# Kernel optimization log

Hardware: AMD Instinct MI355X
Metric: run time of the kernel (lower is better)

Reference implementation:

```python
import jax, jax.numpy as jnp
import numpy as np

B, S, H, NH = 2, 2048, 2048, 16
HD = H // NH
SCALE = 1.0 / np.sqrt(HD).astype(np.float32)


def setup_inputs() -> dict:
    key = jax.random.key(0)
    ks = jax.random.split(key, 10)
    std = 1.0 / np.sqrt(H)
    return {
        "x": jax.random.normal(ks[0], (B, S, H), dtype=jnp.float32),
        "attention_mask": jnp.zeros((B, 1, 1, S), dtype=jnp.float32),
        "Wq": jax.random.normal(ks[1], (H, H), dtype=jnp.float32) * std,
        "bq": jnp.zeros((H,), dtype=jnp.float32),
        "Wk": jax.random.normal(ks[2], (H, H), dtype=jnp.float32) * std,
        "bk": jnp.zeros((H,), dtype=jnp.float32),
        "Wv": jax.random.normal(ks[3], (H, H), dtype=jnp.float32) * std,
        "bv": jnp.zeros((H,), dtype=jnp.float32),
        "Wo": jax.random.normal(ks[4], (H, H), dtype=jnp.float32) * std,
        "bo": jnp.zeros((H,), dtype=jnp.float32),
    }


def _heads(t):
    # [B,S,H] -> [B,NH,S,HD]
    return t.reshape(B, S, NH, HD).transpose(0, 2, 1, 3)


def reference(x, attention_mask, Wq, bq, Wk, bk, Wv, bv, Wo, bo):
    q = _heads(x @ Wq.T + bq)
    k = _heads(x @ Wk.T + bk)
    v = _heads(x @ Wv.T + bv)
    scores = jnp.einsum("bhqd,bhkd->bhqk", q, k) * SCALE + attention_mask
    probs = jax.nn.softmax(scores, axis=-1)
    ctx = jnp.einsum("bhqk,bhkd->bhqd", probs, v)
    ctx = ctx.transpose(0, 2, 1, 3).reshape(B, S, H)
    return ctx @ Wo.T + bo
```

## Files before the change

kernel.cpp:

```cpp
#include <hip/hip_runtime.h>
#include <cstdint>
#include <cstddef>

#define B_   2
#define S_   2048
#define H_   2048
#define NH_  16
#define HD_  128
#define MM_  (B_ * S_)
#define K_   H_
#define SCALE_F 0.08838834764831845f
#define LOG2E_F 1.4426950408889634f
#define QSCALE_F (SCALE_F * LOG2E_F)

typedef __bf16 bf16_t;
typedef __attribute__((ext_vector_type(8))) __bf16 bf16x8;
typedef __attribute__((ext_vector_type(4))) float  f32x4;
typedef __attribute__((ext_vector_type(4))) float  floatx4;

static __device__ __forceinline__ f32x4 mfma_16x16x32(bf16x8 a, bf16x8 b, f32x4 c) {
  return __builtin_amdgcn_mfma_f32_16x16x32_bf16(a, b, c, 0, 0, 0);
}

static __device__ __forceinline__ void gl2lds16(const bf16_t* g, bf16_t* l) {
  __builtin_amdgcn_global_load_lds(
      (const __attribute__((address_space(1))) void*)g,
      (__attribute__((address_space(3))) void*)l, 16, 0, 0);
}

static __device__ __forceinline__ float exp2_hw(float x) {
  float r;
  asm("v_exp_f32 %0, %1" : "=v"(r) : "v"(x));
  return r;
}

__global__ void cvt6_f32_bf16(const float* __restrict__ x,
                              const float* __restrict__ w0, const float* __restrict__ w1,
                              const float* __restrict__ w2, const float* __restrict__ w3,
                              bf16_t* xo, bf16_t* o0, bf16_t* o1, bf16_t* o2, bf16_t* o3,
                              int n8) {
  const int yy = blockIdx.y;
  const float* in;
  bf16_t* out;
  if (yy == 0)      { in = x;                      out = xo; }
  else if (yy == 1) { in = x + (size_t)H_ * H_;    out = xo + (size_t)H_ * H_; }
  else if (yy == 2) { in = w0; out = o0; }
  else if (yy == 3) { in = w1; out = o1; }
  else if (yy == 4) { in = w2; out = o2; }
  else              { in = w3; out = o3; }
  int i = blockIdx.x * blockDim.x + threadIdx.x;
  const int stride = gridDim.x * blockDim.x;
  for (; i < n8; i += stride) {
    const floatx4* p = (const floatx4*)(in + (size_t)i * 8);
    floatx4 a = p[0], b = p[1];
    bf16x8 o;
    o[0] = (bf16_t)a.x; o[1] = (bf16_t)a.y; o[2] = (bf16_t)a.z; o[3] = (bf16_t)a.w;
    o[4] = (bf16_t)b.x; o[5] = (bf16_t)b.y; o[6] = (bf16_t)b.z; o[7] = (bf16_t)b.w;
    *(bf16x8*)(out + (size_t)i * 8) = o;
  }
}

template <int MODE, int NCOLS>
__global__ __launch_bounds__(256) void gemm_bt(
    const bf16_t* __restrict__ A,
    const bf16_t* __restrict__ W0, const bf16_t* __restrict__ W1, const bf16_t* __restrict__ W2,
    const float* __restrict__ bias0, const float* __restrict__ bias1, const float* __restrict__ bias2,
    bf16_t* __restrict__ dq, bf16_t* __restrict__ dk, bf16_t* __restrict__ dv,
    float* __restrict__ outf)
{
  __shared__ __align__(16) bf16_t Ash[128 * 32];
  __shared__ __align__(16) bf16_t Bsh[128 * 32];

  const int t = threadIdx.x;
  const int lane = t & 63;
  const int wid  = t >> 6;
  const int wm = wid >> 1, wn = wid & 1;

  const int lin = blockIdx.x;
  const int xcd = lin & 7;
  const int loc = lin >> 3;
  const int sr  = loc >> 5;
  const int l   = loc & 31;
  const int r_  = xcd * (NCOLS / 8) + sr;
  const int tm  = (r_ & 3) * 8 + (l & 7);
  const int nc  = (r_ >> 2) * 4 + (l >> 3);
  const int bm  = tm * 128;

  int bn;
  int wsel = 0;
  const bf16_t* Bw;
  const float*  bias;
  bf16_t* dsth = nullptr;
  if constexpr (MODE == 0) {
    wsel = nc >> 4;
    bn   = (nc & 15) * 128;
    Bw   = (wsel == 0) ? W0 : ((wsel == 1) ? W1 : W2);
    bias = (wsel == 0) ? bias0 : ((wsel == 1) ? bias1 : bias2);
    dsth = (wsel == 0) ? dq : ((wsel == 1) ? dk : dv);
  } else {
    bn = nc * 128;
    Bw = W0; bias = bias0;
  }

  const bf16_t* gA = A  + (size_t)(bm + (t >> 2)) * K_ + (t & 3) * 8;
  const bf16_t* gB = Bw + (size_t)(bn + (t >> 2)) * K_ + (t & 3) * 8;
  bf16_t* lA = Ash + wid * 512;
  bf16_t* lB = Bsh + wid * 512;

  f32x4 acc[4][4] = {};

  #pragma unroll 1
  for (int k0 = 0; k0 < K_; k0 += 32) {
    gl2lds16(gA + k0,                    lA);
    gl2lds16(gA + k0 + (size_t)64 * K_,  lA + 2048);
    gl2lds16(gB + k0,                    lB);
    gl2lds16(gB + k0 + (size_t)64 * K_,  lB + 2048);
    __syncthreads();

    bf16x8 af[4], bfr[4];
    #pragma unroll
    for (int i = 0; i < 4; ++i) {
      af[i]  = *(const bf16x8*)&Ash[(wm * 64 + i * 16 + (lane & 15)) * 32 + (lane >> 4) * 8];
      bfr[i] = *(const bf16x8*)&Bsh[(wn * 64 + i * 16 + (lane & 15)) * 32 + (lane >> 4) * 8];
    }
    __builtin_amdgcn_s_setprio(1);
    #pragma unroll
    for (int i = 0; i < 4; ++i)
      #pragma unroll
      for (int j = 0; j < 4; ++j)
        acc[i][j] = mfma_16x16x32(af[i], bfr[j], acc[i][j]);
    __builtin_amdgcn_s_setprio(0);
    __syncthreads();
  }

  const int row0 = bm + wm * 64 + (lane >> 4) * 4;
  const int col0 = bn + wn * 64 + (lane & 15);
  #pragma unroll
  for (int j = 0; j < 4; ++j) {
    const int col = col0 + j * 16;
    const float bv = bias[col];
    #pragma unroll
    for (int i = 0; i < 4; ++i) {
      #pragma unroll
      for (int r = 0; r < 4; ++r) {
        const int row = row0 + i * 16 + r;
        float v = acc[i][j][r] + bv;
        if constexpr (MODE == 0) {
          const int ss = row & (S_ - 1);
          const int dd = col & (HD_ - 1);
          const size_t bh = (size_t)((row >> 11) * NH_ + (col >> 7));
          if (wsel == 0) v *= QSCALE_F;
          size_t idx;
          if (wsel == 2) {
            const size_t t1 = bh * 32 + (ss >> 6);
            const size_t t2 = t1 * 8 + (dd >> 4);
            const size_t t3 = t2 * 2 + ((ss >> 5) & 1);
            const size_t ln = (size_t)((dd & 15) | (((ss >> 3) & 3) << 4));
            idx = (t3 * 64 + ln) * 8 + (size_t)(ss & 7);
          } else {
            const size_t t1 = bh * 128 + (ss >> 4);
            const size_t t2 = t1 * 4 + (dd >> 5);
            const size_t ln = (size_t)((ss & 15) | (((dd >> 3) & 3) << 4));
            idx = (t2 * 64 + ln) * 8 + (size_t)(dd & 7);
          }
          dsth[idx] = (bf16_t)v;
        } else {
          outf[(size_t)row * H_ + col] = v;
        }
      }
    }
  }
}

#define KVB 64
#define NT_ (S_ / KVB)
#define TILE_E 8192

__global__ __launch_bounds__(256, 2) void attn_kernel(
    const bf16_t* __restrict__ Qf, const bf16_t* __restrict__ Kf,
    const bf16_t* __restrict__ Vf, const float* __restrict__ mask,
    bf16_t* __restrict__ ctx)
{
  __shared__ __align__(16) bf16_t Klds[TILE_E];
  __shared__ __align__(16) bf16_t Vlds[TILE_E];
  __shared__ __align__(16) bf16_t Plds[4][32 * KVB];

  const int t = threadIdx.x;
  const int lane = t & 63;
  const int wid  = t >> 6;

  const int orig = blockIdx.x;
  const int wg = (orig & 7) * 64 + (orig >> 3);
  const int qt = wg & 15;
  const int bh = wg >> 4;
  const int b  = bh >> 4;
  const int h  = bh & 15;
  const int q0 = qt * 128 + wid * 32;

  const bf16_t* Kh0 = Kf + (size_t)bh * (NT_ * TILE_E);
  const bf16_t* Vh0 = Vf + (size_t)bh * (NT_ * TILE_E);
  const float*  mg  = mask + (size_t)b * S_;

  const bf16_t* Qt = Qf + (((size_t)bh * 128 + (q0 >> 4)) * 4) * 512;
  bf16x8 qf[2][4];
  #pragma unroll
  for (int mh = 0; mh < 2; ++mh)
    #pragma unroll
    for (int ks = 0; ks < 4; ++ks)
      qf[mh][ks] = *(const bf16x8*)&Qt[((mh * 4 + ks) * 64 + lane) * 8];

  f32x4 acc[2][8] = {};
  float m_run[2][4], l_run[2][4];
  #pragma unroll
  for (int mh = 0; mh < 2; ++mh)
    #pragma unroll
    for (int r = 0; r < 4; ++r) { m_run[mh][r] = -INFINITY; l_run[mh][r] = 0.0f; }

  char* Pw = (char*)&Plds[wid][0];

  #pragma unroll 1
  for (int it = 0; it < NT_; ++it) {
    {
      const bf16_t* Ksrc = Kh0 + (size_t)it * TILE_E;
      const bf16_t* Vsrc = Vh0 + (size_t)it * TILE_E;
      #pragma unroll
      for (int i = 0; i < 4; ++i) {
        const int base = (i * 256 + wid * 64) * 8;
        gl2lds16(Ksrc + base + lane * 8, &Klds[base]);
        gl2lds16(Vsrc + base + lane * 8, &Vlds[base]);
      }
    }
    __syncthreads();

    f32x4 sacc[2][4] = {};
    #pragma unroll
    for (int ns = 0; ns < 4; ++ns) {
      #pragma unroll
      for (int ks = 0; ks < 4; ++ks) {
        const bf16x8 kf = *(const bf16x8*)&Klds[((ns * 4 + ks) * 64 + lane) * 8];
        __builtin_amdgcn_s_setprio(1);
        sacc[0][ns] = mfma_16x16x32(qf[0][ks], kf, sacc[0][ns]);
        sacc[1][ns] = mfma_16x16x32(qf[1][ks], kf, sacc[1][ns]);
        __builtin_amdgcn_s_setprio(0);
      }
    }

    const int kv0 = it * KVB;
    float msk[4];
    #pragma unroll
    for (int ns = 0; ns < 4; ++ns)
      msk[ns] = mg[kv0 + ns * 16 + (lane & 15)] * LOG2E_F;

    float sv[2][4][4], tmax[2][4];
    #pragma unroll
    for (int mh = 0; mh < 2; ++mh) {
      #pragma unroll
      for (int r = 0; r < 4; ++r) tmax[mh][r] = -INFINITY;
      #pragma unroll
      for (int ns = 0; ns < 4; ++ns)
        #pragma unroll
        for (int r = 0; r < 4; ++r) {
          sv[mh][ns][r] = sacc[mh][ns][r] + msk[ns];
          tmax[mh][r] = fmaxf(tmax[mh][r], sv[mh][ns][r]);
        }
      #pragma unroll
      for (int off = 1; off < 16; off <<= 1)
        #pragma unroll
        for (int r = 0; r < 4; ++r)
          tmax[mh][r] = fmaxf(tmax[mh][r], __shfl_xor(tmax[mh][r], off));
    }

    bool small = true;
    #pragma unroll
    for (int mh = 0; mh < 2; ++mh)
      #pragma unroll
      for (int r = 0; r < 4; ++r)
        small = small && (tmax[mh][r] <= m_run[mh][r] + 8.0f);
    if (!__all(small)) {
      float scl[2][4];
      #pragma unroll
      for (int mh = 0; mh < 2; ++mh)
        #pragma unroll
        for (int r = 0; r < 4; ++r) {
          const float mnew = fmaxf(m_run[mh][r], tmax[mh][r]);
          scl[mh][r] = exp2_hw(m_run[mh][r] - mnew);
          m_run[mh][r] = mnew;
          l_run[mh][r] *= scl[mh][r];
        }
      #pragma unroll
      for (int mh = 0; mh < 2; ++mh)
        #pragma unroll
        for (int ds = 0; ds < 8; ++ds)
          #pragma unroll
          for (int r = 0; r < 4; ++r)
            acc[mh][ds][r] *= scl[mh][r];
    }

    float rsum[2][4] = {};
    #pragma unroll
    for (int mh = 0; mh < 2; ++mh)
      #pragma unroll
      for (int ns = 0; ns < 4; ++ns)
        #pragma unroll
        for (int r = 0; r < 4; ++r) {
          const float p = exp2_hw(sv[mh][ns][r] - m_run[mh][r]);
          rsum[mh][r] += p;
          const int qq = mh * 16 + (lane >> 4) * 4 + r;
          const int pb = (qq << 7) + ((((ns << 5) | ((lane & 15) << 1))) ^ ((qq & 7) << 4));
          *(bf16_t*)(Pw + pb) = (bf16_t)p;
        }

    bf16x8 pf[2][2];
    #pragma unroll
    for (int mh = 0; mh < 2; ++mh)
      #pragma unroll
      for (int k2 = 0; k2 < 2; ++k2) {
        const int qq = mh * 16 + (lane & 15);
        const int pb = (qq << 7) + (((k2 << 6) | ((lane >> 4) << 4)) ^ ((qq & 7) << 4));
        pf[mh][k2] = *(const bf16x8*)(Pw + pb);
      }

    #pragma unroll
    for (int ds = 0; ds < 8; ++ds) {
      const bf16x8 vf0 = *(const bf16x8*)&Vlds[((ds * 2 + 0) * 64 + lane) * 8];
      const bf16x8 vf1 = *(const bf16x8*)&Vlds[((ds * 2 + 1) * 64 + lane) * 8];
      __builtin_amdgcn_s_setprio(1);
      #pragma unroll
      for (int mh = 0; mh < 2; ++mh) {
        acc[mh][ds] = mfma_16x16x32(pf[mh][0], vf0, acc[mh][ds]);
        acc[mh][ds] = mfma_16x16x32(pf[mh][1], vf1, acc[mh][ds]);
      }
      __builtin_amdgcn_s_setprio(0);
    }

    #pragma unroll
    for (int mh = 0; mh < 2; ++mh)
      #pragma unroll
      for (int off = 1; off < 16; off <<= 1)
        #pragma unroll
        for (int r = 0; r < 4; ++r)
          rsum[mh][r] += __shfl_xor(rsum[mh][r], off);
    #pragma unroll
    for (int mh = 0; mh < 2; ++mh)
      #pragma unroll
      for (int r = 0; r < 4; ++r)
        l_run[mh][r] += rsum[mh][r];

    __syncthreads();
  }

  #pragma unroll
  for (int mh = 0; mh < 2; ++mh)
    #pragma unroll
    for (int ds = 0; ds < 8; ++ds)
      #pragma unroll
      for (int r = 0; r < 4; ++r) {
        const int q = q0 + mh * 16 + (lane >> 4) * 4 + r;
        const int d = ds * 16 + (lane & 15);
        ctx[((size_t)(b * S_ + q)) * H_ + h * HD_ + d] =
            (bf16_t)(acc[mh][ds][r] / l_run[mh][r]);
      }
}

extern "C" void kernel_launch(void* const* d_in, const int* in_sizes, int n_in,
                              void* d_out, int out_size, void* d_ws, size_t ws_size,
                              hipStream_t stream) {
  (void)in_sizes; (void)n_in; (void)out_size; (void)ws_size;
  const float* x    = (const float*)d_in[0];
  const float* mask = (const float*)d_in[1];
  const float* Wq   = (const float*)d_in[2];
  const float* bq   = (const float*)d_in[3];
  const float* Wk   = (const float*)d_in[4];
  const float* bk   = (const float*)d_in[5];
  const float* Wv   = (const float*)d_in[6];
  const float* bv   = (const float*)d_in[7];
  const float* Wo   = (const float*)d_in[8];
  const float* bo   = (const float*)d_in[9];
  float* out = (float*)d_out;

  const size_t nX = (size_t)MM_ * H_;
  const size_t nW = (size_t)H_ * H_;

  bf16_t* xbf = (bf16_t*)d_ws;
  bf16_t* wqb = xbf + nX;
  bf16_t* wkb = wqb + nW;
  bf16_t* wvb = wkb + nW;
  bf16_t* wob = wvb + nW;
  bf16_t* qf  = wob + nW;
  bf16_t* kf  = qf + nX;
  bf16_t* vf  = kf + nX;
  bf16_t* cxb = vf + nX;

  cvt6_f32_bf16<<<dim3(512, 6), 256, 0, stream>>>(
      x, Wq, Wk, Wv, Wo, xbf, wqb, wkb, wvb, wob, (int)(nW / 8));

  gemm_bt<0, 48><<<32 * 48, 256, 0, stream>>>(
      xbf, wqb, wkb, wvb, bq, bk, bv, qf, kf, vf, nullptr);

  attn_kernel<<<512, 256, 0, stream>>>(qf, kf, vf, mask, cxb);

  gemm_bt<1, 16><<<32 * 16, 256, 0, stream>>>(
      cxb, wob, nullptr, nullptr, bo, nullptr, nullptr, nullptr, nullptr, nullptr, out);
}
```

Baseline: 338.0 us.

## Load K and V fragments directly from global memory, dropping LDS staging and barriers

The attention kernel no longer stages K/V tiles through shared memory with block-wide barriers. Each wave reads its MFMA K and V fragments straight from global memory, relying on the pre-swizzled layout and L2/L1 caching, and prefetches the V fragments into registers before the softmax. This removes LDS traffic and the two __syncthreads per iteration. In exchange, each of the four waves re-reads the same K/V tiles from cache, global load latency is exposed, and register pressure rises from holding 16 V fragments.

New measurement: 394.2 us. 1.17x slower.

```diff
diff --git a/kernel.cpp b/kernel.cpp
--- a/kernel.cpp
+++ b/kernel.cpp
@@ -181,8 +181,6 @@
     const bf16_t* __restrict__ Vf, const float* __restrict__ mask,
     bf16_t* __restrict__ ctx)
 {
-  __shared__ __align__(16) bf16_t Klds[TILE_E];
-  __shared__ __align__(16) bf16_t Vlds[TILE_E];
   __shared__ __align__(16) bf16_t Plds[4][32 * KVB];
 
   const int t = threadIdx.x;
@@ -220,30 +218,31 @@
 
   #pragma unroll 1
   for (int it = 0; it < NT_; ++it) {
-    {
-      const bf16_t* Ksrc = Kh0 + (size_t)it * TILE_E;
-      const bf16_t* Vsrc = Vh0 + (size_t)it * TILE_E;
-      #pragma unroll
-      for (int i = 0; i < 4; ++i) {
-        const int base = (i * 256 + wid * 64) * 8;
-        gl2lds16(Ksrc + base + lane * 8, &Klds[base]);
-        gl2lds16(Vsrc + base + lane * 8, &Vlds[base]);
-      }
-    }
-    __syncthreads();
+    const bf16_t* Kt = Kh0 + (size_t)it * TILE_E;
+    const bf16_t* Vt = Vh0 + (size_t)it * TILE_E;
 
     f32x4 sacc[2][4] = {};
     #pragma unroll
     for (int ns = 0; ns < 4; ++ns) {
+      bf16x8 kfv[4];
+      #pragma unroll
+      for (int ks = 0; ks < 4; ++ks)
+        kfv[ks] = *(const bf16x8*)&Kt[((ns * 4 + ks) * 64 + lane) * 8];
+      __builtin_amdgcn_s_setprio(1);
       #pragma unroll
       for (int ks = 0; ks < 4; ++ks) {
-        const bf16x8 kf = *(const bf16x8*)&Klds[((ns * 4 + ks) * 64 + lane) * 8];
-        __builtin_amdgcn_s_setprio(1);
-        sacc[0][ns] = mfma_16x16x32(qf[0][ks], kf, sacc[0][ns]);
-        sacc[1][ns] = mfma_16x16x32(qf[1][ks], kf, sacc[1][ns]);
-        __builtin_amdgcn_s_setprio(0);
-      }
-    }
+        sacc[0][ns] = mfma_16x16x32(qf[0][ks], kfv[ks], sacc[0][ns]);
+        sacc[1][ns] = mfma_16x16x32(qf[1][ks], kfv[ks], sacc[1][ns]);
+      }
+      __builtin_amdgcn_s_setprio(0);
+    }
+
+    bf16x8 vf[8][2];
+    #pragma unroll
+    for (int ds = 0; ds < 8; ++ds)
+      #pragma unroll
+      for (int k2 = 0; k2 < 2; ++k2)
+        vf[ds][k2] = *(const bf16x8*)&Vt[((ds * 2 + k2) * 64 + lane) * 8];
 
     const int kv0 = it * KVB;
     float msk[4];
@@ -322,13 +321,11 @@
 
     #pragma unroll
     for (int ds = 0; ds < 8; ++ds) {
-      const bf16x8 vf0 = *(const bf16x8*)&Vlds[((ds * 2 + 0) * 64 + lane) * 8];
-      const bf16x8 vf1 = *(const bf16x8*)&Vlds[((ds * 2 + 1) * 64 + lane) * 8];
       __builtin_amdgcn_s_setprio(1);
       #pragma unroll
       for (int mh = 0; mh < 2; ++mh) {
-        acc[mh][ds] = mfma_16x16x32(pf[mh][0], vf0, acc[mh][ds]);
-        acc[mh][ds] = mfma_16x16x32(pf[mh][1], vf1, acc[mh][ds]);
+        acc[mh][ds] = mfma_16x16x32(pf[mh][0], vf[ds][0], acc[mh][ds]);
+        acc[mh][ds] = mfma_16x16x32(pf[mh][1], vf[ds][1], acc[mh][ds]);
       }
       __builtin_amdgcn_s_setprio(0);
     }
@@ -345,8 +342,6 @@
       #pragma unroll
       for (int r = 0; r < 4; ++r)
         l_run[mh][r] += rsum[mh][r];
-
-    __syncthreads();
   }
 
   #pragma unroll
```

## Halve attention query tile per wave and double grid for occupancy

Applied to the files above, without the earlier changes.

Each wave now handles 16 query rows instead of 32, so a workgroup covers 64 queries and the grid doubles to 1024 blocks. Launch bounds rise to 4 waves-per-SIMD occupancy and the P scratch buffer shrinks, which cuts register and LDS use per block. The aim is more resident waves and better load balance across CUs, to hide the K/V load latency. The cost is that every K/V tile is loaded from global memory twice as often, and there is less MFMA work per LDS tile, so reuse drops.

After: 348.6 us. 1.03x slower.

```diff
diff --git a/kernel.cpp b/kernel.cpp
--- a/kernel.cpp
+++ b/kernel.cpp
@@ -176,71 +176,68 @@
 #define NT_ (S_ / KVB)
 #define TILE_E 8192
 
-__global__ __launch_bounds__(256, 2) void attn_kernel(
+__global__ __launch_bounds__(256, 4) void attn_kernel(
     const bf16_t* __restrict__ Qf, const bf16_t* __restrict__ Kf,
     const bf16_t* __restrict__ Vf, const float* __restrict__ mask,
     bf16_t* __restrict__ ctx)
 {
   __shared__ __align__(16) bf16_t Klds[TILE_E];
   __shared__ __align__(16) bf16_t Vlds[TILE_E];
-  __shared__ __align__(16) bf16_t Plds[4][32 * KVB];
+  __shared__ __align__(16) bf16_t Plds[4][16 * KVB];
 
   const int t = threadIdx.x;
   const int lane = t & 63;
   const int wid  = t >> 6;
 
   const int orig = blockIdx.x;
-  const int wg = (orig & 7) * 64 + (orig >> 3);
-  const int qt = wg & 15;
-  const int bh = wg >> 4;
+  const int wg = (orig & 7) * 128 + (orig >> 3);
+  const int qt = wg & 31;
+  const int bh = wg >> 5;
   const int b  = bh >> 4;
   const int h  = bh & 15;
-  const int q0 = qt * 128 + wid * 32;
+  const int q0 = qt * 64 + wid * 16;
 
   const bf16_t* Kh0 = Kf + (size_t)bh * (NT_ * TILE_E);
   const bf16_t* Vh0 = Vf + (size_t)bh * (NT_ * TILE_E);
   const float*  mg  = mask + (size_t)b * S_;
 
   const bf16_t* Qt = Qf + (((size_t)bh * 128 + (q0 >> 4)) * 4) * 512;
-  bf16x8 qf[2][4];
+  bf16x8 qf[4];
   #pragma unroll
-  for (int mh = 0; mh < 2; ++mh)
-    #pragma unroll
-    for (int ks = 0; ks < 4; ++ks)
-      qf[mh][ks] = *(const bf16x8*)&Qt[((mh * 4 + ks) * 64 + lane) * 8];
-
-  f32x4 acc[2][8] = {};
-  float m_run[2][4], l_run[2][4];
+  for (int ks = 0; ks < 4; ++ks)
+    qf[ks] = *(const bf16x8*)&Qt[(ks * 64 + lane) * 8];
+
+  f32x4 acc[8] = {};
+  float m_run[4], l_run[4];
   #pragma unroll
-  for (int mh = 0; mh < 2; ++mh)
-    #pragma unroll
-    for (int r = 0; r < 4; ++r) { m_run[mh][r] = -INFINITY; l_run[mh][r] = 0.0f; }
+  for (int r = 0; r < 4; ++r) { m_run[r] = -INFINITY; l_run[r] = 0.0f; }
 
   char* Pw = (char*)&Plds[wid][0];
+
+  auto stage = [&](int it) {
+    const bf16_t* Ksrc = Kh0 + (size_t)it * TILE_E;
+    const bf16_t* Vsrc = Vh0 + (size_t)it * TILE_E;
+    #pragma unroll
+    for (int i = 0; i < 4; ++i) {
+      const int base = (i * 256 + wid * 64) * 8;
+      gl2lds16(Ksrc + base + lane * 8, &Klds[base]);
+      gl2lds16(Vsrc + base + lane * 8, &Vlds[base]);
+    }
+  };
 
   #pragma unroll 1
   for (int it = 0; it < NT_; ++it) {
-    {
-      const bf16_t* Ksrc = Kh0 + (size_t)it * TILE_E;
-      const bf16_t* Vsrc = Vh0 + (size_t)it * TILE_E;
-      #pragma unroll
-      for (int i = 0; i < 4; ++i) {
-        const int base = (i * 256 + wid * 64) * 8;
-        gl2lds16(Ksrc + base + lane * 8, &Klds[base]);
-        gl2lds16(Vsrc + base + lane * 8, &Vlds[base]);
-      }
-    }
+    stage(it);
     __syncthreads();
 
-    f32x4 sacc[2][4] = {};
+    f32x4 sacc[4] = {};
     #pragma unroll
     for (int ns = 0; ns < 4; ++ns) {
       #pragma unroll
       for (int ks = 0; ks < 4; ++ks) {
         const bf16x8 kf = *(const bf16x8*)&Klds[((ns * 4 + ks) * 64 + lane) * 8];
         __builtin_amdgcn_s_setprio(1);
-        sacc[0][ns] = mfma_16x16x32(qf[0][ks], kf, sacc[0][ns]);
-        sacc[1][ns] = mfma_16x16x32(qf[1][ks], kf, sacc[1][ns]);
+        sacc[ns] = mfma_16x16x32(qf[ks], kf, sacc[ns]);
         __builtin_amdgcn_s_setprio(0);
       }
     }
@@ -251,115 +248,93 @@
     for (int ns = 0; ns < 4; ++ns)
       msk[ns] = mg[kv0 + ns * 16 + (lane & 15)] * LOG2E_F;
 
-    float sv[2][4][4], tmax[2][4];
-    #pragma unroll
-    for (int mh = 0; mh < 2; ++mh) {
-      #pragma unroll
-      for (int r = 0; r < 4; ++r) tmax[mh][r] = -INFINITY;
-      #pragma unroll
-      for (int ns = 0; ns < 4; ++ns)
-        #pragma unroll
-        for (int r = 0; r < 4; ++r) {
-          sv[mh][ns][r] = sacc[mh][ns][r] + msk[ns];
-          tmax[mh][r] = fmaxf(tmax[mh][r], sv[mh][ns][r]);
-        }
-      #pragma unroll
-      for (int off = 1; off < 16; off <<= 1)
+    float sv[4][4], tmax[4];
+    #pragma unroll
+    for (int r = 0; r < 4; ++r) tmax[r] = -INFINITY;
+    #pragma unroll
+    for (int ns = 0; ns < 4; ++ns)
+      #pragma unroll
+      for (int r = 0; r < 4; ++r) {
+        sv[ns][r] = sacc[ns][r] + msk[ns];
+        tmax[r] = fmaxf(tmax[r], sv[ns][r]);
+      }
+    #pragma unroll
+    for (int off = 1; off < 16; off <<= 1)
+      #pragma unroll
+      for (int r = 0; r < 4; ++r)
+        tmax[r] = fmaxf(tmax[r], __shfl_xor(tmax[r], off));
+
+    bool small = true;
+    #pragma unroll
+    for (int r = 0; r < 4; ++r)
+      small = small && (tmax[r] <= m_run[r] + 8.0f);
+    if (!__all(small)) {
+      float scl[4];
+      #pragma unroll
+      for (int r = 0; r < 4; ++r) {
+        const float mnew = fmaxf(m_run[r], tmax[r]);
+        scl[r] = exp2_hw(m_run[r] - mnew);
+        m_run[r] = mnew;
+        l_run[r] *= scl[r];
+      }
+      #pragma unroll
+      for (int ds = 0; ds < 8; ++ds)
         #pragma unroll
         for (int r = 0; r < 4; ++r)
-          tmax[mh][r] = fmaxf(tmax[mh][r], __shfl_xor(tmax[mh][r], off));
-    }
-
-    bool small = true;
-    #pragma unroll
-    for (int mh = 0; mh < 2; ++mh)
-      #pragma unroll
-      for (int r = 0; r < 4; ++r)
-        small = small && (tmax[mh][r] <= m_run[mh][r] + 8.0f);
-    if (!__all(small)) {
-      float scl[2][4];
-      #pragma unroll
-      for (int mh = 0; mh < 2; ++mh)
-        #pragma unroll
-        for (int r = 0; r < 4; ++r) {
-          const float mnew = fmaxf(m_run[mh][r], tmax[mh][r]);
-          scl[mh][r] = exp2_hw(m_run[mh][r] - mnew);
-          m_run[mh][r] = mnew;
-          l_run[mh][r] *= scl[mh][r];
-        }
-      #pragma unroll
-      for (int mh = 0; mh < 2; ++mh)
-        #pragma unroll
-        for (int ds = 0; ds < 8; ++ds)
-          #pragma unroll
-          for (int r = 0; r < 4; ++r)
-            acc[mh][ds][r] *= scl[mh][r];
-    }
-
-    float rsum[2][4] = {};
-    #pragma unroll
-    for (int mh = 0; mh < 2; ++mh)
-      #pragma unroll
-      for (int ns = 0; ns < 4; ++ns)
-        #pragma unroll
-        for (int r = 0; r < 4; ++r) {
-          const float p = exp2_hw(sv[mh][ns][r] - m_run[mh][r]);
-          rsum[mh][r] += p;
-          const int qq = mh * 16 + (lane >> 4) * 4 + r;
-          const int pb = (qq << 7) + ((((ns << 5) | ((lane & 15) << 1))) ^ ((qq & 7) << 4));
-          *(bf16_t*)(Pw + pb) = (bf16_t)p;
-        }
-
-    bf16x8 pf[2][2];
-    #pragma unroll
-    for (int mh = 0; mh < 2; ++mh)
-      #pragma unroll
-      for (int k2 = 0; k2 < 2; ++k2) {
-        const int qq = mh * 16 + (lane & 15);
-        const int pb = (qq << 7) + (((k2 << 6) | ((lane >> 4) << 4)) ^ ((qq & 7) << 4));
-        pf[mh][k2] = *(const bf16x8*)(Pw + pb);
-      }
+          acc[ds][r] *= scl[r];
+    }
+
+    float rsum[4] = {};
+    #pragma unroll
+    for (int ns = 0; ns < 4; ++ns)
+      #pragma unroll
+      for (int r = 0; r < 4; ++r) {
+        const float p = exp2_hw(sv[ns][r] - m_run[r]);
+        rsum[r] += p;
+        const int qq = (lane >> 4) * 4 + r;
+        const int pb = (qq << 7) + ((((ns << 5) | ((lane & 15) << 1))) ^ ((qq & 7) << 4));
+        *(bf16_t*)(Pw + pb) = (bf16_t)p;
+      }
+
+    bf16x8 pf[2];
+    #pragma unroll
+    for (int k2 = 0; k2 < 2; ++k2) {
+      const int qq = lane & 15;
+      const int pb = (qq << 7) + (((k2 << 6) | ((lane >> 4) << 4)) ^ ((qq & 7) << 4));
+      pf[k2] = *(const bf16x8*)(Pw + pb);
+    }
 
     #pragma unroll
     for (int ds = 0; ds < 8; ++ds) {
       const bf16x8 vf0 = *(const bf16x8*)&Vlds[((ds * 2 + 0) * 64 + lane) * 8];
       const bf16x8 vf1 = *(const bf16x8*)&Vlds[((ds * 2 + 1) * 64 + lane) * 8];
       __builtin_amdgcn_s_setprio(1);
-      #pragma unroll
-      for (int mh = 0; mh < 2; ++mh) {
-        acc[mh][ds] = mfma_16x16x32(pf[mh][0], vf0, acc[mh][ds]);
-        acc[mh][ds] = mfma_16x16x32(pf[mh][1], vf1, acc[mh][ds]);
-      }
+      acc[ds] = mfma_16x16x32(pf[0], vf0, acc[ds]);
+      acc[ds] = mfma_16x16x32(pf[1], vf1, acc[ds]);
       __builtin_amdgcn_s_setprio(0);
     }
 
     #pragma unroll
-    for (int mh = 0; mh < 2; ++mh)
-      #pragma unroll
-      for (int off = 1; off < 16; off <<= 1)
-        #pragma unroll
-        for (int r = 0; r < 4; ++r)
-          rsum[mh][r] += __shfl_xor(rsum[mh][r], off);
-    #pragma unroll
-    for (int mh = 0; mh < 2; ++mh)
+    for (int off = 1; off < 16; off <<= 1)
       #pragma unroll
       for (int r = 0; r < 4; ++r)
-        l_run[mh][r] += rsum[mh][r];
+        rsum[r] += __shfl_xor(rsum[r], off);
+    #pragma unroll
+    for (int r = 0; r < 4; ++r)
+      l_run[r] += rsum[r];
 
     __syncthreads();
   }
 
   #pragma unroll
-  for (int mh = 0; mh < 2; ++mh)
-    #pragma unroll
-    for (int ds = 0; ds < 8; ++ds)
-      #pragma unroll
-      for (int r = 0; r < 4; ++r) {
-        const int q = q0 + mh * 16 + (lane >> 4) * 4 + r;
-        const int d = ds * 16 + (lane & 15);
-        ctx[((size_t)(b * S_ + q)) * H_ + h * HD_ + d] =
-            (bf16_t)(acc[mh][ds][r] / l_run[mh][r]);
-      }
+  for (int ds = 0; ds < 8; ++ds)
+    #pragma unroll
+    for (int r = 0; r < 4; ++r) {
+      const int q = q0 + (lane >> 4) * 4 + r;
+      const int d = ds * 16 + (lane & 15);
+      ctx[((size_t)(b * S_ + q)) * H_ + h * HD_ + d] =
+          (bf16_t)(acc[ds][r] / l_run[r]);
+    }
 }
 
 extern "C" void kernel_launch(void* const* d_in, const int* in_sizes, int n_in,
@@ -397,7 +372,7 @@
   gemm_bt<0, 48><<<32 * 48, 256, 0, stream>>>(
       xbf, wqb, wkb, wvb, bq, bk, bv, qf, kf, vf, nullptr);
 
-  attn_kernel<<<512, 256, 0, stream>>>(qf, kf, vf, mask, cxb);
+  attn_kernel<<<1024, 256, 0, stream>>>(qf, kf, vf, mask, cxb);
 
   gemm_bt<1, 16><<<32 * 16, 256, 0, stream>>>(
       cxb, wob, nullptr, nullptr, bo, nullptr, nullptr, nullptr, nullptr, nullptr, out);
```
